# Performance work log

Hardware: AMD Instinct MI355X
Metric: run time of the kernel (lower is better)

The kernel has to match this reference:

```python
import jax, jax.numpy as jnp
import numpy as np

B, S, D, H = 2, 1024, 1024, 16
DK, DV = 64, 64
E, F, K = 8, 2048, 2
FSH = 2 * F  # n_shared_experts * moe_inter_dim


def layernorm(x, w, eps=1e-8):
    # RMSNormLayer actually calls F.layer_norm(x, [dim], weight, None, eps)
    mu = jnp.mean(x, axis=-1, keepdims=True)
    var = jnp.mean((x - mu) ** 2, axis=-1, keepdims=True)
    return (x - mu) * jax.lax.rsqrt(var + eps) * w


def _forward(start_pos, x, mask, pos_embedding, attn_norm_w, ffn_norm_w,
             wq, bq, wk, bk, wv, bv, wo, bo, gate_w, gate_b,
             ew1, eb1, ew2, eb2, ew3, eb3, sw1, sb1, sw2, sb2, sw3, sb3):
    b, s, d = x.shape
    # --- attention sublayer ---
    xn = layernorm(x, attn_norm_w)
    q = (xn @ wq + bq).reshape(b, s, H, DK)
    k = (xn @ wk + bk).reshape(b, s, H, DK)
    v = (xn @ wv + bv).reshape(b, s, H, DV)
    score = jnp.einsum('bshk,bShk->bhsS', q, k) / np.float32(np.sqrt(DK))
    pe = pos_embedding[:, start_pos:start_pos + s, start_pos:start_pos + s]  # [H,s,s]
    score = score + pe[None, :, :, :] + mask[:s, :s]
    attn = jax.nn.softmax(score, axis=-1)
    o = jnp.einsum('bhsS,bShv->bshv', attn, v).reshape(b, s, H * DV)
    x = x + o @ wo + bo
    # --- MoE sublayer (eval-path math: y[t] = sum_k w[t,k]*expert_{idx[t,k]}(x[t])) ---
    hn = layernorm(x, ffn_norm_w)
    flat = hn.reshape(-1, d)  # [T, D]
    logits = flat @ gate_w.T + gate_b
    scores = jax.nn.softmax(logits, axis=-1)
    topk_w, topk_idx = jax.lax.top_k(scores, K)
    topk_w = topk_w / (jnp.sum(topk_w, axis=-1, keepdims=True) + 1e-20)
    # per-token per-expert combine weight [T, E]
    comb = jnp.sum(jax.nn.one_hot(topk_idx, E, dtype=flat.dtype) * topk_w[..., None], axis=1)
    # all experts densely (small E), SwiGLU per expert
    a = jnp.einsum('td,edf->tef', flat, ew1) + eb1
    g = jnp.einsum('td,edf->tef', flat, ew3) + eb3
    mid = jax.nn.silu(a) * g
    ye = jnp.einsum('tef,efd->ted', mid, ew2) + eb2  # [T, E, D]
    y = jnp.einsum('te,ted->td', comb, ye)
    # shared experts MLP on the normed input
    shared = (jax.nn.silu(flat @ sw1 + sb1) * (flat @ sw3 + sb3)) @ sw2 + sb2
    return x + (y + shared).reshape(b, s, d)


def setup_inputs() -> dict:
    key = jax.random.key(0)
    ks = jax.random.split(key, 16)
    def rn(i, shape, s=0.02):
        return jax.random.normal(ks[i], shape, jnp.float32) * s
    return dict(
        x=rn(0, (B, S, D), 1.0),
        start_pos=0,
        mask=jnp.zeros((S, S), jnp.float32),
        pos_embedding=rn(1, (H, S, S)),
        attn_norm_w=jnp.ones((D,), jnp.float32),
        ffn_norm_w=jnp.ones((D,), jnp.float32),
        wq=rn(2, (D, H * DK)), bq=jnp.zeros((H * DK,), jnp.float32),
        wk=rn(3, (D, H * DK)), bk=jnp.zeros((H * DK,), jnp.float32),
        wv=rn(4, (D, H * DV)), bv=jnp.zeros((H * DV,), jnp.float32),
        wo=rn(5, (H * DV, D)), bo=jnp.zeros((D,), jnp.float32),
        gate_w=rn(6, (E, D), 1.0), gate_b=rn(7, (E,), 1.0),
        ew1=rn(8, (E, D, F)), eb1=jnp.zeros((E, F), jnp.float32),
        ew2=rn(9, (E, F, D)), eb2=jnp.zeros((E, D), jnp.float32),
        ew3=rn(10, (E, D, F)), eb3=jnp.zeros((E, F), jnp.float32),
        sw1=rn(11, (D, FSH)), sb1=jnp.zeros((FSH,), jnp.float32),
        sw2=rn(12, (FSH, D)), sb2=jnp.zeros((D,), jnp.float32),
        sw3=rn(13, (D, FSH)), sb3=jnp.zeros((FSH,), jnp.float32),
    )


def reference(x, start_pos, mask, pos_embedding, attn_norm_w, ffn_norm_w,
              wq, bq, wk, bk, wv, bv, wo, bo, gate_w, gate_b,
              ew1, eb1, ew2, eb2, ew3, eb3, sw1, sb1, sw2, sb2, sw3, sb3):
    return _forward(start_pos, x, mask, pos_embedding, attn_norm_w, ffn_norm_w,
                    wq, bq, wk, bk, wv, bv, wo, bo, gate_w, gate_b,
                    ew1, eb1, ew2, eb2, ew3, eb3, sw1, sb1, sw2, sb2, sw3, sb3)
```

## Files before the change

kernel.cpp:

```cpp
#include <hip/hip_runtime.h>
#include <hip/hip_bf16.h>

#define BB 2
#define SS 1024
#define DD 1024
#define HH 16
#define DKV 64
#define EE 8
#define FF 2048
#define FSH2 4096

typedef __attribute__((ext_vector_type(8))) short bf16x8;
typedef __attribute__((ext_vector_type(4))) float f32x4;

#define EPI_PLAIN 0
#define EPI_SCATTER 2
#define AM_DENSE 0
#define AM_GATHER 1
#define AM_GROUP 2

__device__ inline unsigned pack_bf2(float lo, float hi) {
    __hip_bfloat162 h = __float22bfloat162_rn(float2{lo, hi});
    union { __hip_bfloat162 h2; unsigned u; } c; c.h2 = h; return c.u;
}
__device__ inline unsigned short bf16_1(float x) {
    union { __hip_bfloat16 b; unsigned short u; } c;
    c.b = __float2bfloat16(x); return c.u;
}

#define LOADT(s, k0) {                                                        \
    const float4* ap4 = (const float4*)(Ap + (k0));                           \
    pa##s##_0 = ap4[0]; pa##s##_1 = ap4[1];                                   \
    pa##s##_2 = ap4[2]; pa##s##_3 = ap4[3];                                   \
    const float* wp = Wcol + (size_t)((k0) + kg * 8) * N;                     \
    _Pragma("unroll")                                                         \
    for (int j = 0; j < 8; ++j) pb##s[j] = wp[(size_t)j * N];                 \
}
#define STAGET(s) {                                                           \
    uint4 aw0, aw1;                                                           \
    aw0.x = pack_bf2(pa##s##_0.x, pa##s##_0.y);                               \
    aw0.y = pack_bf2(pa##s##_0.z, pa##s##_0.w);                               \
    aw0.z = pack_bf2(pa##s##_1.x, pa##s##_1.y);                               \
    aw0.w = pack_bf2(pa##s##_1.z, pa##s##_1.w);                               \
    aw1.x = pack_bf2(pa##s##_2.x, pa##s##_2.y);                               \
    aw1.y = pack_bf2(pa##s##_2.z, pa##s##_2.w);                               \
    aw1.z = pack_bf2(pa##s##_3.x, pa##s##_3.y);                               \
    aw1.w = pack_bf2(pa##s##_3.z, pa##s##_3.w);                               \
    *(uint4*)&As[ar * 40 + ac] = aw0;                                         \
    *(uint4*)&As[ar * 40 + ac + 8] = aw1;                                     \
    uint4 bw;                                                                 \
    bw.x = pack_bf2(pb##s[0], pb##s[1]);  bw.y = pack_bf2(pb##s[2], pb##s[3]);\
    bw.z = pack_bf2(pb##s[4], pb##s[5]);  bw.w = pack_bf2(pb##s[6], pb##s[7]);\
    *(uint4*)&Bs[bn * 32 + slB * 8] = bw;                                     \
}
#define MFMAT() {                                                             \
    bf16x8 af[4], bfr[2];                                                     \
    _Pragma("unroll")                                                         \
    for (int m = 0; m < 4; ++m) {                                             \
        int row = wr * 64 + m * 16 + ll;                                      \
        af[m] = *(const bf16x8*)&As[row * 40 + lh * 8];                       \
    }                                                                         \
    _Pragma("unroll")                                                         \
    for (int n = 0; n < 2; ++n) {                                             \
        int col = wc * 32 + n * 16 + ll;                                      \
        int slot = lh ^ (col & 3);                                            \
        bfr[n] = *(const bf16x8*)&Bs[col * 32 + slot * 8];                    \
    }                                                                         \
    _Pragma("unroll")                                                         \
    for (int m = 0; m < 4; ++m)                                               \
        _Pragma("unroll")                                                     \
        for (int n = 0; n < 2; ++n)                                           \
            acc[m][n] = __builtin_amdgcn_mfma_f32_16x16x32_bf16(af[m], bfr[n], acc[m][n], 0, 0, 0); \
}
#define PHASET(s, nx) {                                                       \
    STAGET(s)                                                                 \
    if ((nx) < NT) LOADT(s, (nx) << 5)                                        \
    asm volatile("s_waitcnt lgkmcnt(0)\n\ts_barrier" ::: "memory");           \
    MFMAT()                                                                   \
    asm volatile("s_barrier" ::: "memory");                                   \
}

template<int EPI, int AMODE, int NSEL, int SPLITK>
__global__ __launch_bounds__(256, 2) void mgemm(
    const float* __restrict__ A,
    const float* __restrict__ W0, const float* __restrict__ W1p, const float* __restrict__ W2p,
    const float* __restrict__ b0, const float* __restrict__ b1p, const float* __restrict__ b2p,
    const float* __restrict__ addsrc,
    float* __restrict__ C0, float* __restrict__ C1p, float* __restrict__ C2p,
    int M, int N, int K,
    const int* __restrict__ tok_list, const int* __restrict__ cnt,
    const int* __restrict__ offs, const float* __restrict__ comb,
    const int* __restrict__ idx0, float* __restrict__ y1)
{
    __shared__ __align__(16) unsigned short As[128 * 40];
    __shared__ __align__(16) unsigned short Bs[64 * 32];
    __shared__ int rows_s[128];
    const int t = threadIdx.x;
    const float* W = W0; const float* bias = b0; float* C = C0;
    if (NSEL == 3) {
        if (blockIdx.z == 1) { W = W1p; bias = b1p; C = C1p; }
        else if (blockIdx.z == 2) { W = W2p; bias = b2p; C = C2p; }
    }
    const int e = (AMODE != AM_DENSE) ? blockIdx.z : 0;
    int ne = M, base = 0;
    if (AMODE != AM_DENSE) {
        ne = cnt[e];
        base = offs[e];
        if ((int)blockIdx.y * 128 >= ne) return;
        W += (size_t)e * K * N;
        bias += (size_t)e * N;
    }
    const int m0 = blockIdx.y * 128;
    const int n0 = blockIdx.x * 64;
    if (AMODE == AM_GATHER) {
        if (t < 128) {
            int li = m0 + t; if (li >= ne) li = ne - 1;
            rows_s[t] = tok_list[e * 2048 + li];
        }
        __syncthreads();
    }
    const int ar = t >> 1;
    const int ac = (t & 1) * 16;
    const int bn = t & 63;
    const int kg = t >> 6;
    const int slB = kg ^ (bn & 3);
    long arow;
    if (AMODE == AM_DENSE) arow = m0 + ar;
    else if (AMODE == AM_GATHER) arow = rows_s[ar];
    else { int li = m0 + ar; if (li >= ne) li = ne - 1; arow = base + li; }
    const int Kc = (SPLITK > 1) ? (K / SPLITK) : K;
    const size_t koff = (SPLITK > 1) ? (size_t)blockIdx.z * Kc : 0;
    const float* Ap = A + (size_t)arow * K + ac + koff;
    const float* Wcol = W + koff * N + n0 + bn;
    const int l = t & 63, w = t >> 6;
    const int wr = w >> 1, wc = w & 1;
    const int lh = l >> 4, ll = l & 15;
    f32x4 acc[4][2];
#pragma unroll
    for (int i = 0; i < 4; ++i)
#pragma unroll
        for (int j = 0; j < 2; ++j) acc[i][j] = f32x4{0.f, 0.f, 0.f, 0.f};

    const int NT = Kc >> 5;
    float4 pa0_0, pa0_1, pa0_2, pa0_3; float pb0[8];
    float4 pa1_0, pa1_1, pa1_2, pa1_3; float pb1[8];
    float4 pa2_0, pa2_1, pa2_2, pa2_3; float pb2[8];
    float4 pa3_0, pa3_1, pa3_2, pa3_3; float pb3[8];
    LOADT(0, 0)
    LOADT(1, 32)
    LOADT(2, 64)
    LOADT(3, 96)
    for (int it = 0; it < NT; it += 4) {
        PHASET(0, it + 4)
        PHASET(1, it + 5)
        PHASET(2, it + 6)
        PHASET(3, it + 7)
    }

#pragma unroll
    for (int m = 0; m < 4; ++m) {
#pragma unroll
        for (int n = 0; n < 2; ++n) {
            int colg = n0 + wc * 32 + n * 16 + ll;
            float bvv = (SPLITK > 1) ? 0.f : bias[colg];
#pragma unroll
            for (int j = 0; j < 4; ++j) {
                int li = m0 + wr * 64 + m * 16 + lh * 4 + j;
                float v = acc[m][n][j] + bvv;
                if (SPLITK > 1) {
                    C[(size_t)blockIdx.z * M * N + (size_t)li * N + colg] = v;
                } else if (EPI == EPI_PLAIN) {
                    if (AMODE == AM_DENSE) {
                        if (addsrc) v += addsrc[(size_t)li * N + colg];
                        C[(size_t)li * N + colg] = v;
                    } else {
                        if (li < ne) C[(size_t)(base + li) * N + colg] = v;
                    }
                } else {
                    if (li < ne) {
                        int tok = tok_list[e * 2048 + li];
                        float wgt = comb[tok * 8 + e];
                        float* dst = (idx0[tok] == e) ? C : y1;
                        dst[(size_t)tok * N + colg] = wgt * v;
                    }
                }
            }
        }
    }
}

#define LOAD2T(s, k0) {                                                       \
    const float4* ap4 = (const float4*)(Ap + (k0));                           \
    pa##s##_0 = ap4[0]; pa##s##_1 = ap4[1];                                   \
    pa##s##_2 = ap4[2]; pa##s##_3 = ap4[3];                                   \
    const float* wp1 = W1col + (size_t)((k0) + kg * 8) * N;                   \
    const float* wp3 = W3col + (size_t)((k0) + kg * 8) * N;                   \
    _Pragma("unroll")                                                         \
    for (int j = 0; j < 8; ++j) {                                             \
        pb1##s[j] = wp1[(size_t)j * N];                                       \
        pb3##s[j] = wp3[(size_t)j * N];                                       \
    }                                                                         \
}
#define STAGE2T(s) {                                                          \
    uint4 aw0, aw1;                                                           \
    aw0.x = pack_bf2(pa##s##_0.x, pa##s##_0.y);                               \
    aw0.y = pack_bf2(pa##s##_0.z, pa##s##_0.w);                               \
    aw0.z = pack_bf2(pa##s##_1.x, pa##s##_1.y);                               \
    aw0.w = pack_bf2(pa##s##_1.z, pa##s##_1.w);                               \
    aw1.x = pack_bf2(pa##s##_2.x, pa##s##_2.y);                               \
    aw1.y = pack_bf2(pa##s##_2.z, pa##s##_2.w);                               \
    aw1.z = pack_bf2(pa##s##_3.x, pa##s##_3.y);                               \
    aw1.w = pack_bf2(pa##s##_3.z, pa##s##_3.w);                               \
    *(uint4*)&As[ar * 40 + ac] = aw0;                                         \
    *(uint4*)&As[ar * 40 + ac + 8] = aw1;                                     \
    uint4 bw;                                                                 \
    bw.x = pack_bf2(pb1##s[0], pb1##s[1]);  bw.y = pack_bf2(pb1##s[2], pb1##s[3]); \
    bw.z = pack_bf2(pb1##s[4], pb1##s[5]);  bw.w = pack_bf2(pb1##s[6], pb1##s[7]); \
    *(uint4*)&B1s[bn * 32 + slB * 8] = bw;                                    \
    bw.x = pack_bf2(pb3##s[0], pb3##s[1]);  bw.y = pack_bf2(pb3##s[2], pb3##s[3]); \
    bw.z = pack_bf2(pb3##s[4], pb3##s[5]);  bw.w = pack_bf2(pb3##s[6], pb3##s[7]); \
    *(uint4*)&B3s[bn * 32 + slB * 8] = bw;                                    \
}
#define MFMA2T() {                                                            \
    bf16x8 af[4], bfr[2];                                                     \
    _Pragma("unroll")                                                         \
    for (int m = 0; m < 4; ++m) {                                             \
        int row = wr * 64 + m * 16 + ll;                                      \
        af[m] = *(const bf16x8*)&As[row * 40 + lh * 8];                       \
    }                                                                         \
    _Pragma("unroll")                                                         \
    for (int n = 0; n < 2; ++n) {                                             \
        int col = wc * 32 + n * 16 + ll;                                      \
        int slot = lh ^ (col & 3);                                            \
        bfr[n] = *(const bf16x8*)&B1s[col * 32 + slot * 8];                   \
    }                                                                         \
    _Pragma("unroll")                                                         \
    for (int m = 0; m < 4; ++m)                                               \
        _Pragma("unroll")                                                     \
        for (int n = 0; n < 2; ++n)                                           \
            acc1[m][n] = __builtin_amdgcn_mfma_f32_16x16x32_bf16(af[m], bfr[n], acc1[m][n], 0, 0, 0); \
    _Pragma("unroll")                                                         \
    for (int n = 0; n < 2; ++n) {                                             \
        int col = wc * 32 + n * 16 + ll;                                      \
        int slot = lh ^ (col & 3);                                            \
        bfr[n] = *(const bf16x8*)&B3s[col * 32 + slot * 8];                   \
    }                                                                         \
    _Pragma("unroll")                                                         \
    for (int m = 0; m < 4; ++m)                                               \
        _Pragma("unroll")                                                     \
        for (int n = 0; n < 2; ++n)                                           \
            acc3[m][n] = __builtin_amdgcn_mfma_f32_16x16x32_bf16(af[m], bfr[n], acc3[m][n], 0, 0, 0); \
}
#define PHASE2T(s, nx) {                                                      \
    STAGE2T(s)                                                                \
    if ((nx) < NT) LOAD2T(s, (nx) << 5)                                       \
    asm volatile("s_waitcnt lgkmcnt(0)\n\ts_barrier" ::: "memory");           \
    MFMA2T()                                                                  \
    asm volatile("s_barrier" ::: "memory");                                   \
}

template<int AMODE>
__global__ __launch_bounds__(256, 2) void mgemm2(
    const float* __restrict__ A,
    const float* __restrict__ W1, const float* __restrict__ W3,
    const float* __restrict__ B1, const float* __restrict__ B3,
    float* __restrict__ Out, int M, int N, int K,
    const int* __restrict__ tok_list, const int* __restrict__ cnt,
    const int* __restrict__ offs)
{
    __shared__ __align__(16) unsigned short As[128 * 40];
    __shared__ __align__(16) unsigned short B1s[64 * 32];
    __shared__ __align__(16) unsigned short B3s[64 * 32];
    __shared__ int rows_s[128];
    const int t = threadIdx.x;
    const int e = (AMODE == AM_GATHER) ? blockIdx.z : 0;
    int ne = M, base = 0;
    const float *w1 = W1, *w3 = W3, *b1 = B1, *b3 = B3;
    if (AMODE == AM_GATHER) {
        ne = cnt[e];
        base = offs[e];
        if ((int)blockIdx.y * 128 >= ne) return;
        w1 += (size_t)e * K * N; w3 += (size_t)e * K * N;
        b1 += (size_t)e * N;     b3 += (size_t)e * N;
    }
    const int m0 = blockIdx.y * 128;
    const int n0 = blockIdx.x * 64;
    if (AMODE == AM_GATHER) {
        if (t < 128) {
            int li = m0 + t; if (li >= ne) li = ne - 1;
            rows_s[t] = tok_list[e * 2048 + li];
        }
        __syncthreads();
    }
    const int ar = t >> 1;
    const int ac = (t & 1) * 16;
    const int bn = t & 63;
    const int kg = t >> 6;
    const int slB = kg ^ (bn & 3);
    long arow = (AMODE == AM_GATHER) ? (long)rows_s[ar] : (long)(m0 + ar);
    const float* Ap = A + (size_t)arow * K + ac;
    const float* W1col = w1 + n0 + bn;
    const float* W3col = w3 + n0 + bn;
    const int l = t & 63, w = t >> 6;
    const int wr = w >> 1, wc = w & 1;
    const int lh = l >> 4, ll = l & 15;
    f32x4 acc1[4][2], acc3[4][2];
#pragma unroll
    for (int i = 0; i < 4; ++i)
#pragma unroll
        for (int j = 0; j < 2; ++j) {
            acc1[i][j] = f32x4{0.f, 0.f, 0.f, 0.f};
            acc3[i][j] = f32x4{0.f, 0.f, 0.f, 0.f};
        }
    const int NT = K >> 5;
    float4 pa0_0, pa0_1, pa0_2, pa0_3; float pb10[8], pb30[8];
    float4 pa1_0, pa1_1, pa1_2, pa1_3; float pb11[8], pb31[8];
    LOAD2T(0, 0)
    LOAD2T(1, 32)
    for (int it = 0; it < NT; it += 2) {
        PHASE2T(0, it + 2)
        PHASE2T(1, it + 3)
    }
#pragma unroll
    for (int m = 0; m < 4; ++m) {
#pragma unroll
        for (int n = 0; n < 2; ++n) {
            int colg = n0 + wc * 32 + n * 16 + ll;
            float bv1 = b1[colg], bv3 = b3[colg];
#pragma unroll
            for (int j = 0; j < 4; ++j) {
                int li = m0 + wr * 64 + m * 16 + lh * 4 + j;
                if (AMODE == AM_GATHER && li >= ne) continue;
                float a = acc1[m][n][j] + bv1;
                float g = acc3[m][n][j] + bv3;
                float sil = a / (1.0f + __expf(-a));
                size_t off = (AMODE == AM_GATHER) ? (size_t)(base + li) * N + colg
                                                  : (size_t)li * N + colg;
                Out[off] = sil * g;
            }
        }
    }
}

__global__ __launch_bounds__(256) void reducek(const float* __restrict__ P, int ns,
                                               const float* __restrict__ bias,
                                               const float* __restrict__ addsrc,
                                               float* __restrict__ out, int N) {
    size_t i = (size_t)blockIdx.x * 256 + threadIdx.x;
    const size_t MN4 = (size_t)2048 * N / 4;
    float4 s = ((const float4*)P)[i];
    for (int sl = 1; sl < ns; ++sl) {
        float4 p = ((const float4*)P)[i + (size_t)sl * MN4];
        s.x += p.x; s.y += p.y; s.z += p.z; s.w += p.w;
    }
    int col4 = (int)(i & ((N >> 2) - 1));
    float4 b = ((const float4*)bias)[col4];
    s.x += b.x; s.y += b.y; s.z += b.z; s.w += b.w;
    if (addsrc) {
        float4 a = ((const float4*)addsrc)[i];
        s.x += a.x; s.y += a.y; s.z += a.z; s.w += a.w;
    }
    ((float4*)out)[i] = s;
}

__global__ __launch_bounds__(256) void ln_kernel(const float* __restrict__ x,
                                                 const float* __restrict__ w,
                                                 float* __restrict__ y) {
    __shared__ float red[4], red2[4];
    const int row = blockIdx.x;
    const int t = threadIdx.x;
    const float4* xr = (const float4*)(x + (size_t)row * DD);
    float4 v = xr[t];
    float s = v.x + v.y + v.z + v.w;
    float q = v.x * v.x + v.y * v.y + v.z * v.z + v.w * v.w;
    for (int o = 32; o; o >>= 1) { s += __shfl_down(s, o); q += __shfl_down(q, o); }
    if ((t & 63) == 0) { red[t >> 6] = s; red2[t >> 6] = q; }
    __syncthreads();
    float S = red[0] + red[1] + red[2] + red[3];
    float Q = red2[0] + red2[1] + red2[2] + red2[3];
    float mu = S * (1.0f / DD);
    float var = Q * (1.0f / DD) - mu * mu;
    float inv = rsqrtf(var + 1e-8f);
    const float4* wr = (const float4*)w;
    float4 wv = wr[t];
    float4 o4;
    o4.x = (v.x - mu) * inv * wv.x;
    o4.y = (v.y - mu) * inv * wv.y;
    o4.z = (v.z - mu) * inv * wv.z;
    o4.w = (v.w - mu) * inv * wv.w;
    ((float4*)(y + (size_t)row * DD))[t] = o4;
}

__global__ __launch_bounds__(256) void attn_mfma(const float* __restrict__ Q,
                                                 const float* __restrict__ Kk,
                                                 const float* __restrict__ V,
                                                 const float* __restrict__ pe,
                                                 const float* __restrict__ mask,
                                                 const int* __restrict__ sp_ptr,
                                                 float* __restrict__ O) {
    __shared__ __align__(16) unsigned short Kt[64 * 64];
    __shared__ __align__(16) unsigned short Vt[64 * 64];
    __shared__ __align__(16) unsigned short Pl[4][16 * 64];
    const int t = threadIdx.x;
    const int w = t >> 6, l = t & 63;
    const int ll = l & 15, lh = l >> 4;
    const int bh = blockIdx.y;
    const int b = bh >> 4, h = bh & 15;
    const int q0 = blockIdx.x * 64;
    const int sp = sp_ptr[0];

    bf16x8 qf[2];
    {
        const float* qp = Q + (size_t)(b * SS + q0 + w * 16 + ll) * DD + h * 64 + lh * 8;
#pragma unroll
        for (int kk = 0; kk < 2; ++kk) {
            float4 x0 = *(const float4*)(qp + kk * 32);
            float4 x1 = *(const float4*)(qp + kk * 32 + 4);
            uint4 u;
            u.x = pack_bf2(x0.x * 0.125f, x0.y * 0.125f);
            u.y = pack_bf2(x0.z * 0.125f, x0.w * 0.125f);
            u.z = pack_bf2(x1.x * 0.125f, x1.y * 0.125f);
            u.w = pack_bf2(x1.z * 0.125f, x1.w * 0.125f);
            qf[kk] = *(bf16x8*)&u;
        }
    }
    f32x4 oacc[4];
#pragma unroll
    for (int n = 0; n < 4; ++n) oacc[n] = f32x4{0.f, 0.f, 0.f, 0.f};
    float mrun[4], lrun[4];
#pragma unroll
    for (int j = 0; j < 4; ++j) { mrun[j] = -3.0e38f; lrun[j] = 0.f; }

    const size_t pebase = (size_t)h * SS * SS + (size_t)sp;

    for (int kt0 = 0; kt0 < SS; kt0 += 64) {
        __syncthreads();
        {
            const int key = t >> 2, dg = (t & 3) * 16;
            const float* kp = Kk + (size_t)(b * SS + kt0 + key) * DD + h * 64 + dg;
            float4 k0 = *(const float4*)kp, k1 = *(const float4*)(kp + 4);
            float4 k2 = *(const float4*)(kp + 8), k3 = *(const float4*)(kp + 12);
            uint4 u0, u1;
            u0.x = pack_bf2(k0.x, k0.y); u0.y = pack_bf2(k0.z, k0.w);
            u0.z = pack_bf2(k1.x, k1.y); u0.w = pack_bf2(k1.z, k1.w);
            u1.x = pack_bf2(k2.x, k2.y); u1.y = pack_bf2(k2.z, k2.w);
            u1.z = pack_bf2(k3.x, k3.y); u1.w = pack_bf2(k3.z, k3.w);
            const int sw = (key & 7) << 4;
            *(uint4*)((char*)Kt + key * 128 + ((dg * 2) ^ sw)) = u0;
            *(uint4*)((char*)Kt + key * 128 + ((dg * 2 + 16) ^ sw)) = u1;
        }
        {
            const int kp2 = t & 31, vg = (t >> 5) * 8;
            const float* vp0 = V + (size_t)(b * SS + kt0 + 2 * kp2) * DD + h * 64 + vg;
            const float* vp1 = vp0 + DD;
            float4 a0 = *(const float4*)vp0, a1 = *(const float4*)(vp0 + 4);
            float4 b0 = *(const float4*)vp1, b1 = *(const float4*)(vp1 + 4);
            float va[8] = {a0.x, a0.y, a0.z, a0.w, a1.x, a1.y, a1.z, a1.w};
            float vb[8] = {b0.x, b0.y, b0.z, b0.w, b1.x, b1.y, b1.z, b1.w};
#pragma unroll
            for (int j = 0; j < 8; ++j) {
                int vd = vg + j;
                unsigned u = pack_bf2(va[j], vb[j]);
                *(unsigned*)((char*)Vt + vd * 128 + ((kp2 * 4) ^ ((vd & 7) << 4))) = u;
            }
        }
        __syncthreads();
        f32x4 sc[4];
#pragma unroll
        for (int n = 0; n < 4; ++n) sc[n] = f32x4{0.f, 0.f, 0.f, 0.f};
#pragma unroll
        for (int n = 0; n < 4; ++n) {
            const int key = n * 16 + ll;
            const int sw = (key & 7) << 4;
#pragma unroll
            for (int kk = 0; kk < 2; ++kk) {
                bf16x8 kf = *(const bf16x8*)((char*)Kt + key * 128 + ((kk * 64 + lh * 16) ^ sw));
                sc[n] = __builtin_amdgcn_mfma_f32_16x16x32_bf16(qf[kk], kf, sc[n], 0, 0, 0);
            }
        }
#pragma unroll
        for (int j = 0; j < 4; ++j) {
            const int qrow = q0 + w * 16 + lh * 4 + j;
            const float* per = pe + pebase + (size_t)(sp + qrow) * SS + kt0 + ll;
            const float* mar = mask + (size_t)qrow * SS + kt0 + ll;
#pragma unroll
            for (int n = 0; n < 4; ++n)
                sc[n][j] += per[n * 16] + mar[n * 16];
        }
#pragma unroll
        for (int j = 0; j < 4; ++j) {
            float mx = fmaxf(fmaxf(sc[0][j], sc[1][j]), fmaxf(sc[2][j], sc[3][j]));
#pragma unroll
            for (int o = 1; o < 16; o <<= 1) mx = fmaxf(mx, __shfl_xor(mx, o));
            float mnew = fmaxf(mrun[j], mx);
            float corr = __expf(mrun[j] - mnew);
            mrun[j] = mnew;
            float ssum = 0.f;
#pragma unroll
            for (int n = 0; n < 4; ++n) {
                float p = __expf(sc[n][j] - mnew);
                sc[n][j] = p;
                ssum += p;
            }
#pragma unroll
            for (int o = 1; o < 16; o <<= 1) ssum += __shfl_xor(ssum, o);
            lrun[j] = lrun[j] * corr + ssum;
#pragma unroll
            for (int n = 0; n < 4; ++n) oacc[n][j] *= corr;
        }
#pragma unroll
        for (int j = 0; j < 4; ++j) {
            const int lq = lh * 4 + j;
            const int sw = (lq & 7) << 4;
#pragma unroll
            for (int n = 0; n < 4; ++n) {
                const int key = n * 16 + ll;
                *(unsigned short*)((char*)Pl[w] + lq * 128 + ((key * 2) ^ sw)) =
                    bf16_1(sc[n][j]);
            }
        }
        asm volatile("s_waitcnt lgkmcnt(0)" ::: "memory");
        __builtin_amdgcn_sched_barrier(0);
#pragma unroll
        for (int kk = 0; kk < 2; ++kk) {
            const int lq = ll;
            bf16x8 pf = *(const bf16x8*)((char*)Pl[w] + lq * 128 +
                                         ((kk * 64 + lh * 16) ^ ((lq & 7) << 4)));
#pragma unroll
            for (int n = 0; n < 4; ++n) {
                const int vd = n * 16 + ll;
                bf16x8 vf = *(const bf16x8*)((char*)Vt + vd * 128 +
                                             ((kk * 64 + lh * 16) ^ ((vd & 7) << 4)));
                oacc[n] = __builtin_amdgcn_mfma_f32_16x16x32_bf16(pf, vf, oacc[n], 0, 0, 0);
            }
        }
    }
#pragma unroll
    for (int j = 0; j < 4; ++j) {
        const int qrow = q0 + w * 16 + lh * 4 + j;
        const float invl = 1.0f / lrun[j];
#pragma unroll
        for (int n = 0; n < 4; ++n)
            O[(size_t)(b * SS + qrow) * DD + h * 64 + n * 16 + ll] = oacc[n][j] * invl;
    }
}

__global__ __launch_bounds__(64) void gate_kernel(const float* __restrict__ hn,
                                                  const float* __restrict__ gw,
                                                  const float* __restrict__ gb,
                                                  float* __restrict__ comb,
                                                  int* __restrict__ idx0,
                                                  int* __restrict__ cnt,
                                                  int* __restrict__ tok_list) {
    __shared__ float lg[8];
    const int tok = blockIdx.x;
    const int lane = threadIdx.x;
    const int e = lane >> 3, chunk = lane & 7;
    const float* hr = hn + (size_t)tok * DD + chunk * 128;
    const float* gr = gw + (size_t)e * DD + chunk * 128;
    float p = 0.f;
    for (int j = 0; j < 128; ++j) p += hr[j] * gr[j];
    p += __shfl_down(p, 4, 8);
    p += __shfl_down(p, 2, 8);
    p += __shfl_down(p, 1, 8);
    if (chunk == 0) lg[e] = p + gb[e];
    __syncthreads();
    if (lane == 0) {
        float mx = lg[0];
        for (int i = 1; i < 8; ++i) mx = fmaxf(mx, lg[i]);
        float pr[8]; float ssum = 0.f;
        for (int i = 0; i < 8; ++i) { pr[i] = __expf(lg[i] - mx); ssum += pr[i]; }
        float is = 1.0f / ssum;
        for (int i = 0; i < 8; ++i) pr[i] *= is;
        int i1 = 0;
        for (int i = 1; i < 8; ++i) if (pr[i] > pr[i1]) i1 = i;
        int i2 = -1;
        for (int i = 0; i < 8; ++i) { if (i == i1) continue; if (i2 < 0 || pr[i] > pr[i2]) i2 = i; }
        float w0 = pr[i1], w1 = pr[i2];
        float nrm = 1.0f / (w0 + w1 + 1e-20f);
        w0 *= nrm; w1 *= nrm;
        for (int i = 0; i < 8; ++i) comb[tok * 8 + i] = 0.0f;
        comb[tok * 8 + i1] = w0;
        comb[tok * 8 + i2] = w1;
        idx0[tok] = i1;
        int s1 = atomicAdd(&cnt[i1], 1); tok_list[i1 * 2048 + s1] = tok;
        int s2 = atomicAdd(&cnt[i2], 1); tok_list[i2 * 2048 + s2] = tok;
    }
}

__global__ void init_cnt(int* cnt) { if (threadIdx.x < 8) cnt[threadIdx.x] = 0; }

__global__ void prefix_kernel(const int* __restrict__ cnt, int* __restrict__ offs) {
    if (threadIdx.x == 0) {
        int a = 0;
        for (int e = 0; e < 8; ++e) { offs[e] = a; a += cnt[e]; }
    }
}

__global__ __launch_bounds__(256) void final_kernel(const float* __restrict__ x2,
                                                    const float* __restrict__ y0,
                                                    const float* __restrict__ y1,
                                                    const float* __restrict__ sh,
                                                    float* __restrict__ out) {
    size_t i = (size_t)blockIdx.x * 256 + threadIdx.x;
    float4 a = ((const float4*)x2)[i];
    float4 b = ((const float4*)y0)[i];
    float4 c = ((const float4*)y1)[i];
    float4 d = ((const float4*)sh)[i];
    float4 o;
    o.x = a.x + b.x + c.x + d.x;
    o.y = a.y + b.y + c.y + d.y;
    o.z = a.z + b.z + c.z + d.z;
    o.w = a.w + b.w + c.w + d.w;
    ((float4*)out)[i] = o;
}

#define NUL6 nullptr, nullptr, nullptr, nullptr, nullptr, nullptr

extern "C" void kernel_launch(void* const* d_in, const int* in_sizes, int n_in,
                              void* d_out, int out_size, void* d_ws, size_t ws_size,
                              hipStream_t stream) {
    const float* x   = (const float*)d_in[0];
    const int*   sp  = (const int*)d_in[1];
    const float* mask= (const float*)d_in[2];
    const float* pe  = (const float*)d_in[3];
    const float* anw = (const float*)d_in[4];
    const float* fnw = (const float*)d_in[5];
    const float* wq  = (const float*)d_in[6];  const float* bq  = (const float*)d_in[7];
    const float* wk  = (const float*)d_in[8];  const float* bk  = (const float*)d_in[9];
    const float* wv  = (const float*)d_in[10]; const float* bv  = (const float*)d_in[11];
    const float* wo  = (const float*)d_in[12]; const float* bo  = (const float*)d_in[13];
    const float* gw  = (const float*)d_in[14]; const float* gb  = (const float*)d_in[15];
    const float* ew1 = (const float*)d_in[16]; const float* eb1 = (const float*)d_in[17];
    const float* ew2 = (const float*)d_in[18]; const float* eb2 = (const float*)d_in[19];
    const float* ew3 = (const float*)d_in[20]; const float* eb3 = (const float*)d_in[21];
    const float* sw1 = (const float*)d_in[22]; const float* sb1 = (const float*)d_in[23];
    const float* sw2 = (const float*)d_in[24]; const float* sb2 = (const float*)d_in[25];
    const float* sw3 = (const float*)d_in[26]; const float* sb3 = (const float*)d_in[27];

    float* ws = (float*)d_ws;
    const size_t M2 = (size_t)2048 * 1024;
    float* comb = ws;
    int* idx0   = (int*)(ws + 16384);
    int* cnt    = idx0 + 2048;
    int* offs   = cnt + 8;
    int* tok_list = offs + 8;
    float* base = ws + 65536;
    float* xn   = base;
    float* q    = base + 1 * M2;
    float* kbuf = base + 2 * M2;
    float* vbuf = base + 3 * M2;
    float* x2   = base + 4 * M2;
    float* amid = base + 5 * M2;
    float* psw2 = base + 9 * M2;
    const bool big = ws_size >= (size_t)(65536 + 13 * M2) * sizeof(float);
    float* o   = xn;
    float* hn  = q;
    float* y0  = xn;
    float* y1  = kbuf;
    float* sh  = vbuf;

    ln_kernel<<<2048, 256, 0, stream>>>(x, anw, xn);
    mgemm<EPI_PLAIN, AM_DENSE, 3, 1><<<dim3(16, 16, 3), 256, 0, stream>>>(
        xn, wq, wk, wv, bq, bk, bv, nullptr, q, kbuf, vbuf,
        2048, 1024, 1024, NUL6);
    attn_mfma<<<dim3(SS / 64, BB * HH), 256, 0, stream>>>(q, kbuf, vbuf, pe, mask, sp, o);
    mgemm<EPI_PLAIN, AM_DENSE, 1, 4><<<dim3(16, 16, 4), 256, 0, stream>>>(
        o, wo, nullptr, nullptr, bo, nullptr, nullptr, nullptr, amid, nullptr, nullptr,
        2048, 1024, 1024, NUL6);
    reducek<<<2048, 256, 0, stream>>>(amid, 4, bo, x, x2, 1024);
    ln_kernel<<<2048, 256, 0, stream>>>(x2, fnw, hn);
    init_cnt<<<1, 64, 0, stream>>>(cnt);
    gate_kernel<<<2048, 64, 0, stream>>>(hn, gw, gb, comb, idx0, cnt, tok_list);
    prefix_kernel<<<1, 64, 0, stream>>>(cnt, offs);
    mgemm2<AM_GATHER><<<dim3(32, 16, 8), 256, 0, stream>>>(
        hn, ew1, ew3, eb1, eb3, amid, 2048, FF, 1024, tok_list, cnt, offs);
    mgemm<EPI_SCATTER, AM_GROUP, 1, 1><<<dim3(16, 16, 8), 256, 0, stream>>>(
        amid, ew2, nullptr, nullptr, eb2, nullptr, nullptr, nullptr, y0, nullptr, nullptr,
        2048, DD, FF, tok_list, cnt, offs, comb, idx0, y1);
    mgemm2<AM_DENSE><<<dim3(64, 16), 256, 0, stream>>>(
        hn, sw1, sw3, sb1, sb3, amid, 2048, FSH2, 1024, nullptr, nullptr, nullptr);
    if (big) {
        mgemm<EPI_PLAIN, AM_DENSE, 1, 4><<<dim3(16, 16, 4), 256, 0, stream>>>(
            amid, sw2, nullptr, nullptr, sb2, nullptr, nullptr, nullptr, psw2, nullptr, nullptr,
            2048, DD, FSH2, NUL6);
        reducek<<<2048, 256, 0, stream>>>(psw2, 4, sb2, nullptr, sh, 1024);
    } else {
        mgemm<EPI_PLAIN, AM_DENSE, 1, 1><<<dim3(16, 16), 256, 0, stream>>>(
            amid, sw2, nullptr, nullptr, sb2, nullptr, nullptr, nullptr, sh, nullptr, nullptr,
            2048, DD, FSH2, NUL6);
    }
    final_kernel<<<2048, 256, 0, stream>>>(x2, y0, y1, sh, (float*)d_out);
}
```

Before: 572.3 us.

## Merge routed and shared expert up-projection GEMMs into one launch

Adds a combined kernel whose z-slices 0-7 compute the routed experts' gated SwiGLU up-projection and whose slice 8 computes the shared expert's. The two GEMMs run concurrently in one grid, so the shared expert's work fills compute units left idle by empty or partial routed tiles. The shared intermediate now lives in its own workspace buffer, and the partial-sum buffer is reused. This applies only when the workspace is large enough. Many routed blocks exit early because the grid x is sized for the wider shared GEMM.

After: 567.3 us. Within noise of the previous version (-0.9%).

```diff
diff --git a/kernel.cpp b/kernel.cpp
--- a/kernel.cpp
+++ b/kernel.cpp
@@ -257,6 +257,47 @@
     asm volatile("s_waitcnt lgkmcnt(0)\n\ts_barrier" ::: "memory");           \
     MFMA2T()                                                                  \
     asm volatile("s_barrier" ::: "memory");                                   \
+}
+
+#define MGEMM2_BODY(GATED) {                                                  \
+    const int l = t & 63, w = t >> 6;                                         \
+    const int wr = w >> 1, wc = w & 1;                                        \
+    const int lh = l >> 4, ll = l & 15;                                       \
+    f32x4 acc1[4][2], acc3[4][2];                                             \
+    _Pragma("unroll")                                                         \
+    for (int i = 0; i < 4; ++i)                                               \
+        _Pragma("unroll")                                                     \
+        for (int j = 0; j < 2; ++j) {                                         \
+            acc1[i][j] = f32x4{0.f, 0.f, 0.f, 0.f};                           \
+            acc3[i][j] = f32x4{0.f, 0.f, 0.f, 0.f};                           \
+        }                                                                     \
+    const int NT = K >> 5;                                                    \
+    float4 pa0_0, pa0_1, pa0_2, pa0_3; float pb10[8], pb30[8];                \
+    float4 pa1_0, pa1_1, pa1_2, pa1_3; float pb11[8], pb31[8];                \
+    LOAD2T(0, 0)                                                              \
+    LOAD2T(1, 32)                                                             \
+    for (int it = 0; it < NT; it += 2) {                                      \
+        PHASE2T(0, it + 2)                                                    \
+        PHASE2T(1, it + 3)                                                    \
+    }                                                                         \
+    _Pragma("unroll")                                                         \
+    for (int m = 0; m < 4; ++m) {                                             \
+        _Pragma("unroll")                                                     \
+        for (int n = 0; n < 2; ++n) {                                         \
+            int colg = n0 + wc * 32 + n * 16 + ll;                            \
+            float bv1 = b1[colg], bv3 = b3[colg];                             \
+            _Pragma("unroll")                                                 \
+            for (int j = 0; j < 4; ++j) {                                     \
+                int li = m0 + wr * 64 + m * 16 + lh * 4 + j;                  \
+                if (GATED && li >= ne) continue;                              \
+                float a = acc1[m][n][j] + bv1;                                \
+                float g = acc3[m][n][j] + bv3;                                \
+                float sil = a / (1.0f + __expf(-a));                          \
+                size_t off = (size_t)(base + li) * N + colg;                  \
+                Out[off] = sil * g;                                           \
+            }                                                                 \
+        }                                                                     \
+    }                                                                         \
 }
 
 template<int AMODE>
@@ -301,45 +342,64 @@
     const float* Ap = A + (size_t)arow * K + ac;
     const float* W1col = w1 + n0 + bn;
     const float* W3col = w3 + n0 + bn;
-    const int l = t & 63, w = t >> 6;
-    const int wr = w >> 1, wc = w & 1;
-    const int lh = l >> 4, ll = l & 15;
-    f32x4 acc1[4][2], acc3[4][2];
-#pragma unroll
-    for (int i = 0; i < 4; ++i)
-#pragma unroll
-        for (int j = 0; j < 2; ++j) {
-            acc1[i][j] = f32x4{0.f, 0.f, 0.f, 0.f};
-            acc3[i][j] = f32x4{0.f, 0.f, 0.f, 0.f};
-        }
-    const int NT = K >> 5;
-    float4 pa0_0, pa0_1, pa0_2, pa0_3; float pb10[8], pb30[8];
-    float4 pa1_0, pa1_1, pa1_2, pa1_3; float pb11[8], pb31[8];
-    LOAD2T(0, 0)
-    LOAD2T(1, 32)
-    for (int it = 0; it < NT; it += 2) {
-        PHASE2T(0, it + 2)
-        PHASE2T(1, it + 3)
-    }
-#pragma unroll
-    for (int m = 0; m < 4; ++m) {
-#pragma unroll
-        for (int n = 0; n < 2; ++n) {
-            int colg = n0 + wc * 32 + n * 16 + ll;
-            float bv1 = b1[colg], bv3 = b3[colg];
-#pragma unroll
-            for (int j = 0; j < 4; ++j) {
-                int li = m0 + wr * 64 + m * 16 + lh * 4 + j;
-                if (AMODE == AM_GATHER && li >= ne) continue;
-                float a = acc1[m][n][j] + bv1;
-                float g = acc3[m][n][j] + bv3;
-                float sil = a / (1.0f + __expf(-a));
-                size_t off = (AMODE == AM_GATHER) ? (size_t)(base + li) * N + colg
-                                                  : (size_t)li * N + colg;
-                Out[off] = sil * g;
-            }
-        }
-    }
+    if (AMODE == AM_GATHER) { MGEMM2_BODY(1) } else { MGEMM2_BODY(0) }
+}
+
+__global__ __launch_bounds__(256, 2) void mgemm2m(
+    const float* __restrict__ A,
+    const float* __restrict__ W1r, const float* __restrict__ W3r,
+    const float* __restrict__ B1r, const float* __restrict__ B3r,
+    const float* __restrict__ W1sh, const float* __restrict__ W3sh,
+    const float* __restrict__ B1sh, const float* __restrict__ B3sh,
+    float* __restrict__ OutR, float* __restrict__ OutS, int K,
+    const int* __restrict__ tok_list, const int* __restrict__ cnt,
+    const int* __restrict__ offs)
+{
+    __shared__ __align__(16) unsigned short As[128 * 40];
+    __shared__ __align__(16) unsigned short B1s[64 * 32];
+    __shared__ __align__(16) unsigned short B3s[64 * 32];
+    __shared__ int rows_s[128];
+    const int t = threadIdx.x;
+    const int z = blockIdx.z;
+    const bool routed = (z < 8);
+    int N, ne, base;
+    const float *w1, *w3, *b1, *b3;
+    float* Out;
+    if (routed) {
+        if ((int)blockIdx.x >= FF / 64) return;
+        N = FF;
+        ne = cnt[z];
+        base = offs[z];
+        if ((int)blockIdx.y * 128 >= ne) return;
+        w1 = W1r + (size_t)z * K * N; w3 = W3r + (size_t)z * K * N;
+        b1 = B1r + (size_t)z * N;     b3 = B3r + (size_t)z * N;
+        Out = OutR;
+    } else {
+        N = FSH2;
+        ne = 2048;
+        base = 0;
+        w1 = W1sh; w3 = W3sh; b1 = B1sh; b3 = B3sh;
+        Out = OutS;
+    }
+    const int m0 = blockIdx.y * 128;
+    const int n0 = blockIdx.x * 64;
+    if (routed) {
+        if (t < 128) {
+            int li = m0 + t; if (li >= ne) li = ne - 1;
+            rows_s[t] = tok_list[z * 2048 + li];
+        }
+        __syncthreads();
+    }
+    const int ar = t >> 1;
+    const int ac = (t & 1) * 16;
+    const int bn = t & 63;
+    const int kg = t >> 6;
+    const int slB = kg ^ (bn & 3);
+    long arow = routed ? (long)rows_s[ar] : (long)(m0 + ar);
+    const float* Ap = A + (size_t)arow * K + ac;
+    const float* W1col = w1 + n0 + bn;
+    const float* W3col = w3 + n0 + bn;
+    if (routed) { MGEMM2_BODY(1) } else { MGEMM2_BODY(0) }
 }
 
 __global__ __launch_bounds__(256) void reducek(const float* __restrict__ P, int ns,
@@ -652,7 +712,7 @@
     float* vbuf = base + 3 * M2;
     float* x2   = base + 4 * M2;
     float* amid = base + 5 * M2;
-    float* psw2 = base + 9 * M2;
+    float* smid = base + 9 * M2;
     const bool big = ws_size >= (size_t)(65536 + 13 * M2) * sizeof(float);
     float* o   = xn;
     float* hn  = q;
@@ -673,19 +733,26 @@
     init_cnt<<<1, 64, 0, stream>>>(cnt);
     gate_kernel<<<2048, 64, 0, stream>>>(hn, gw, gb, comb, idx0, cnt, tok_list);
     prefix_kernel<<<1, 64, 0, stream>>>(cnt, offs);
-    mgemm2<AM_GATHER><<<dim3(32, 16, 8), 256, 0, stream>>>(
-        hn, ew1, ew3, eb1, eb3, amid, 2048, FF, 1024, tok_list, cnt, offs);
-    mgemm<EPI_SCATTER, AM_GROUP, 1, 1><<<dim3(16, 16, 8), 256, 0, stream>>>(
-        amid, ew2, nullptr, nullptr, eb2, nullptr, nullptr, nullptr, y0, nullptr, nullptr,
-        2048, DD, FF, tok_list, cnt, offs, comb, idx0, y1);
-    mgemm2<AM_DENSE><<<dim3(64, 16), 256, 0, stream>>>(
-        hn, sw1, sw3, sb1, sb3, amid, 2048, FSH2, 1024, nullptr, nullptr, nullptr);
+
     if (big) {
+        mgemm2m<<<dim3(64, 16, 9), 256, 0, stream>>>(
+            hn, ew1, ew3, eb1, eb3, sw1, sw3, sb1, sb3,
+            amid, smid, 1024, tok_list, cnt, offs);
+        mgemm<EPI_SCATTER, AM_GROUP, 1, 1><<<dim3(16, 16, 8), 256, 0, stream>>>(
+            amid, ew2, nullptr, nullptr, eb2, nullptr, nullptr, nullptr, y0, nullptr, nullptr,
+            2048, DD, FF, tok_list, cnt, offs, comb, idx0, y1);
         mgemm<EPI_PLAIN, AM_DENSE, 1, 4><<<dim3(16, 16, 4), 256, 0, stream>>>(
-            amid, sw2, nullptr, nullptr, sb2, nullptr, nullptr, nullptr, psw2, nullptr, nullptr,
+            smid, sw2, nullptr, nullptr, sb2, nullptr, nullptr, nullptr, amid, nullptr, nullptr,
             2048, DD, FSH2, NUL6);
-        reducek<<<2048, 256, 0, stream>>>(psw2, 4, sb2, nullptr, sh, 1024);
+        reducek<<<2048, 256, 0, stream>>>(amid, 4, sb2, nullptr, sh, 1024);
     } else {
+        mgemm2<AM_GATHER><<<dim3(32, 16, 8), 256, 0, stream>>>(
+            hn, ew1, ew3, eb1, eb3, amid, 2048, FF, 1024, tok_list, cnt, offs);
+        mgemm<EPI_SCATTER, AM_GROUP, 1, 1><<<dim3(16, 16, 8), 256, 0, stream>>>(
+            amid, ew2, nullptr, nullptr, eb2, nullptr, nullptr, nullptr, y0, nullptr, nullptr,
+            2048, DD, FF, tok_list, cnt, offs, comb, idx0, y1);
+        mgemm2<AM_DENSE><<<dim3(64, 16), 256, 0, stream>>>(
+            hn, sw1, sw3, sb1, sb3, amid, 2048, FSH2, 1024, nullptr, nullptr, nullptr);
         mgemm<EPI_PLAIN, AM_DENSE, 1, 1><<<dim3(16, 16), 256, 0, stream>>>(
             amid, sw2, nullptr, nullptr, sb2, nullptr, nullptr, nullptr, sh, nullptr, nullptr,
             2048, DD, FSH2, NUL6);
```
